# Performance work log

Measured on AMD Instinct MI355X. Metric: run time of the kernel, lower is better.

## Reference

```python
import jax, jax.numpy as jnp
import numpy as np

E = 1024        # embedding_dim
H = 16          # num_heads
DR = 1          # downsample_rate
INT = E // DR   # internal_dim
HD = INT // H   # head dim
B, NQ, NK = 4, 2048, 2048


def setup_inputs() -> dict:
    key = jax.random.key(0)
    ks = jax.random.split(key, 11)
    s_in = 1.0 / np.sqrt(E)
    s_int = 1.0 / np.sqrt(INT)
    return {
        "q": jax.random.normal(ks[0], (B, NQ, E), jnp.float32),
        "k": jax.random.normal(ks[1], (B, NK, E), jnp.float32),
        "v": jax.random.normal(ks[2], (B, NK, E), jnp.float32),
        "wq": jax.random.normal(ks[3], (E, INT), jnp.float32) * s_in,
        "bq": jnp.zeros((INT,), jnp.float32),
        "wk": jax.random.normal(ks[4], (E, INT), jnp.float32) * s_in,
        "bk": jnp.zeros((INT,), jnp.float32),
        "wv": jax.random.normal(ks[5], (E, INT), jnp.float32) * s_in,
        "bv": jnp.zeros((INT,), jnp.float32),
        "wo": jax.random.normal(ks[6], (INT, E), jnp.float32) * s_int,
        "bo": jnp.zeros((E,), jnp.float32),
    }


def _heads(x):
    # (B, N, INT) -> (B, H, N, HD)
    b, n, c = x.shape
    return x.reshape(b, n, H, c // H).transpose(0, 2, 1, 3)


def reference(q, k, v, wq, bq, wk, bk, wv, bv, wo, bo):
    qh = _heads(q @ wq + bq)          # (B,H,NQ,HD)
    kh = _heads(k @ wk + bk)          # (B,H,NK,HD)
    vh = _heads(v @ wv + bv)          # (B,H,NK,HD)
    scale = 1.0 / np.sqrt(HD)
    attn = jnp.einsum('bhqd,bhkd->bhqk', qh, kh) * scale  # (B,H,NQ,NK)
    attn = jax.nn.softmax(attn, axis=-1)
    out = jnp.einsum('bhqk,bhkd->bhqd', attn, vh)          # (B,H,NQ,HD)
    out = out.transpose(0, 2, 1, 3).reshape(q.shape[0], qh.shape[2], INT)
    return out @ wo + bo
```

## Files before the change

kernel.cpp:

```cpp
#include <hip/hip_runtime.h>
#include <hip/hip_bf16.h>
#include <cstdint>
#include <cstddef>

typedef __bf16 bf16_t;
typedef __bf16 bf16x8 __attribute__((ext_vector_type(8)));
typedef float f32x4 __attribute__((ext_vector_type(4)));
typedef float f32x16 __attribute__((ext_vector_type(16)));
typedef uint32_t u32;

#define EDIM 1024
#define HH 16
#define HD 64
#define NSEQ 2048
#define QSCALE 0.18033688011f

__device__ __forceinline__ void async_copy16(const bf16_t* gsrc, bf16_t* lds_dst) {
    __builtin_amdgcn_global_load_lds(
        (const __attribute__((address_space(1))) uint32_t*)gsrc,
        (__attribute__((address_space(3))) uint32_t*)lds_dst,
        16, 0, 0);
}

__global__ void cvt_f32_bf16(const float* __restrict__ in, bf16_t* __restrict__ out) {
    size_t i = ((size_t)blockIdx.x * 256 + threadIdx.x) * 8;
    float4 x = *(const float4*)(in + i);
    float4 y = *(const float4*)(in + i + 4);
    bf16x8 v = {(bf16_t)x.x, (bf16_t)x.y, (bf16_t)x.z, (bf16_t)x.w,
                (bf16_t)y.x, (bf16_t)y.y, (bf16_t)y.z, (bf16_t)y.w};
    *(bf16x8*)(out + i) = v;
}

__global__ void transpose_all(const float* __restrict__ w0, const float* __restrict__ w1,
                              const float* __restrict__ w2, const float* __restrict__ w3,
                              bf16_t* __restrict__ o0, bf16_t* __restrict__ o1,
                              bf16_t* __restrict__ o2, bf16_t* __restrict__ o3) {
    __shared__ bf16_t t[64][65];
    const float* in;
    bf16_t* out;
    switch (blockIdx.z) {
        case 0: in = w0; out = o0; break;
        case 1: in = w1; out = o1; break;
        case 2: in = w2; out = o2; break;
        default: in = w3; out = o3; break;
    }
    const int tid = threadIdx.x;
    const int kt = blockIdx.x, nt = blockIdx.y;
    #pragma unroll
    for (int i = 0; i < 16; i++) {
        int idx = i * 256 + tid;
        int r = idx >> 6, c = idx & 63;
        t[r][c] = (bf16_t)in[(size_t)(kt * 64 + r) * 1024 + nt * 64 + c];
    }
    __syncthreads();
    #pragma unroll
    for (int i = 0; i < 16; i++) {
        int idx = i * 256 + tid;
        int r = idx >> 6, c = idx & 63;
        out[(size_t)(nt * 64 + r) * 1024 + kt * 64 + c] = t[c][r];
    }
}

template <int AB, int MODE, typename OUT>
__global__ __launch_bounds__(256, 2)
void gemm_nt(const void* __restrict__ Araw, const bf16_t* __restrict__ Bt,
             const float* __restrict__ bias, OUT* __restrict__ C,
             int M, int N, int K, float oscale) {
    constexpr int BM = 128, BN = 128, BK = 32;
    __shared__ bf16_t Asm[BM * BK];
    __shared__ bf16_t Bsm[BN * BK];
    const int tid = threadIdx.x;
    const int wave = tid >> 6, lane = tid & 63;
    const int quad = lane >> 4, l15 = lane & 15;
    const int n0 = blockIdx.x * BN;
    const int m0 = blockIdx.y * BM;
    const int wm = (wave & 1) * 64, wn = (wave >> 1) * 64;

    f32x4 acc[4][4] = {};

    for (int k0 = 0; k0 < K; k0 += BK) {
        __syncthreads();
        if (AB) {
            const bf16_t* A = (const bf16_t*)Araw;
            #pragma unroll
            for (int i = 0; i < 2; i++) {
                int s = i * 256 + tid;
                int row = s >> 2, c = s & 3;
                int kc = c ^ ((row >> 1) & 3);
                async_copy16(A + (size_t)(m0 + row) * K + k0 + kc * 8, Asm + s * 8);
            }
        } else {
            const float* A = (const float*)Araw;
            #pragma unroll
            for (int i = 0; i < 2; i++) {
                int s = i * 256 + tid;
                int row = s >> 2, c = s & 3;
                int kc = c ^ ((row >> 1) & 3);
                const float* sp = A + (size_t)(m0 + row) * K + k0 + kc * 8;
                float4 x = *(const float4*)sp;
                float4 y = *(const float4*)(sp + 4);
                bf16x8 vv = {(bf16_t)x.x, (bf16_t)x.y, (bf16_t)x.z, (bf16_t)x.w,
                             (bf16_t)y.x, (bf16_t)y.y, (bf16_t)y.z, (bf16_t)y.w};
                *(bf16x8*)&Asm[s * 8] = vv;
            }
        }
        #pragma unroll
        for (int i = 0; i < 2; i++) {
            int s = i * 256 + tid;
            int row = s >> 2, c = s & 3;
            int kc = c ^ ((row >> 1) & 3);
            async_copy16(Bt + (size_t)(n0 + row) * K + k0 + kc * 8, Bsm + s * 8);
        }
        __syncthreads();

        bf16x8 af[4], bfr[4];
        #pragma unroll
        for (int mi = 0; mi < 4; mi++) {
            int row = wm + mi * 16 + l15;
            af[mi] = *(const bf16x8*)&Asm[row * BK + ((quad ^ ((row >> 1) & 3)) * 8)];
        }
        #pragma unroll
        for (int ni = 0; ni < 4; ni++) {
            int row = wn + ni * 16 + l15;
            bfr[ni] = *(const bf16x8*)&Bsm[row * BK + ((quad ^ ((row >> 1) & 3)) * 8)];
        }
        #pragma unroll
        for (int mi = 0; mi < 4; mi++)
            #pragma unroll
            for (int ni = 0; ni < 4; ni++)
                acc[mi][ni] = __builtin_amdgcn_mfma_f32_16x16x32_bf16(
                    af[mi], bfr[ni], acc[mi][ni], 0, 0, 0);
    }

    #pragma unroll
    for (int mi = 0; mi < 4; mi++) {
        #pragma unroll
        for (int ni = 0; ni < 4; ni++) {
            #pragma unroll
            for (int r = 0; r < 4; r++) {
                int m = m0 + wm + mi * 16 + quad * 4 + r;
                int nch = n0 + wn + ni * 16 + l15;
                float v = (acc[mi][ni][r] + bias[nch]) * oscale;
                if (MODE == 2) {
                    C[(size_t)m * N + nch] = (OUT)v;
                } else {
                    int b = m >> 11, n = m & 2047;
                    int h = nch >> 6, d = nch & 63;
                    if (MODE == 0)
                        C[(((size_t)(b * HH + h)) * NSEQ + n) * HD + d] = (OUT)v;
                    else
                        C[(((size_t)(b * HH + h)) * HD + d) * NSEQ + n] = (OUT)v;
                }
            }
        }
    }
}

union PW { u32 w[4]; bf16x8 v; };

__device__ __forceinline__ u32 pack_bf16(float lo, float hi) {
    union { bf16_t h[2]; u32 u; } x;
    x.h[0] = (bf16_t)lo;
    x.h[1] = (bf16_t)hi;
    return x.u;
}

__device__ __forceinline__ void half_swap(u32& a, u32& b, int hi) {
    u32 as = (u32)__shfl_xor((int)a, 32, 64);
    u32 bs = (u32)__shfl_xor((int)b, 32, 64);
    a = hi ? bs : a;
    b = hi ? b : as;
}

__device__ __forceinline__ void softmax_pack(const f32x16 sa, float* lp, int hi,
                                             PW& f0, PW& f1) {
    float p[16];
    #pragma unroll
    for (int r = 0; r < 16; r++) {
        p[r] = exp2f(sa[r]);
        lp[r & 3] += p[r];
    }
    u32 x0 = pack_bf16(p[0],  p[1]),  x1 = pack_bf16(p[2],  p[3]);
    u32 x2 = pack_bf16(p[4],  p[5]),  x3 = pack_bf16(p[6],  p[7]);
    u32 x4 = pack_bf16(p[8],  p[9]),  x5 = pack_bf16(p[10], p[11]);
    u32 x6 = pack_bf16(p[12], p[13]), x7 = pack_bf16(p[14], p[15]);
    half_swap(x0, x2, hi); half_swap(x1, x3, hi);
    half_swap(x4, x6, hi); half_swap(x5, x7, hi);
    f0.w[0] = x0; f0.w[1] = x1; f0.w[2] = x2; f0.w[3] = x3;
    f1.w[0] = x4; f1.w[1] = x5; f1.w[2] = x6; f1.w[3] = x7;
}

__global__ __launch_bounds__(256, 4)
void attn_kernel(const bf16_t* __restrict__ Qh, const bf16_t* __restrict__ Kh,
                 const bf16_t* __restrict__ Vt, bf16_t* __restrict__ out) {
    __shared__ bf16_t Ks[2][64 * 64];
    __shared__ bf16_t Vs[2][64 * 64];
    const int tid = threadIdx.x, wave = tid >> 6, lane = tid & 63;
    const int l31 = lane & 31, hi = lane >> 5;
    const int B = blockIdx.x;
    const int qt = (B >> 3) & 15;
    const int bh = (B >> 7) * 8 + (B & 7);
    const int b = bh >> 4, h = bh & 15;

    const bf16_t* kbase = Kh + (size_t)bh * NSEQ * HD;
    const bf16_t* vbase = Vt + (size_t)bh * HD * NSEQ;

    bf16x8 qf[4];
    {
        const bf16_t* qrow =
            Qh + ((size_t)bh * NSEQ + qt * 128 + wave * 32 + l31) * HD + hi * 8;
        #pragma unroll
        for (int s = 0; s < 4; s++) qf[s] = *(const bf16x8*)(qrow + s * 16);
    }

    const bf16_t *ks0, *ks1, *vs0, *vs1;
    {
        int r0 = tid >> 3, c0 = tid & 7;
        int s1 = tid + 256;
        int r1 = s1 >> 3, c1 = s1 & 7;
        ks0 = kbase + r0 * HD + (c0 ^ (r0 & 7)) * 8;
        ks1 = kbase + r1 * HD + (c1 ^ (r1 & 7)) * 8;
        vs0 = vbase + (size_t)r0 * NSEQ + (c0 ^ (r0 & 7)) * 8;
        vs1 = vbase + (size_t)r1 * NSEQ + (c1 ^ (r1 & 7)) * 8;
    }

    async_copy16(ks0, &Ks[0][tid * 8]);
    async_copy16(ks1, &Ks[0][(tid + 256) * 8]);
    async_copy16(vs0, &Vs[0][tid * 8]);
    async_copy16(vs1, &Vs[0][(tid + 256) * 8]);

    f32x16 oacc[2] = {};
    float lp[4] = {};

    for (int t = 0; t < 32; t++) {
        const int cur = t & 1;
        __syncthreads();

        if (t < 31) {
            ks0 += 64 * HD; ks1 += 64 * HD;
            vs0 += 64;      vs1 += 64;
            async_copy16(ks0, &Ks[cur ^ 1][tid * 8]);
            async_copy16(ks1, &Ks[cur ^ 1][(tid + 256) * 8]);
            async_copy16(vs0, &Vs[cur ^ 1][tid * 8]);
            async_copy16(vs1, &Vs[cur ^ 1][(tid + 256) * 8]);
        }

        f32x16 sacc0 = {};
        f32x16 sacc1 = {};
        #pragma unroll
        for (int s = 0; s < 4; s++) {
            int g = s * 2 + hi;
            int row0 = l31;
            int row1 = 32 + l31;
            bf16x8 ak0 = *(const bf16x8*)&Ks[cur][row0 * 64 + ((g ^ (row0 & 7)) * 8)];
            bf16x8 ak1 = *(const bf16x8*)&Ks[cur][row1 * 64 + ((g ^ (row1 & 7)) * 8)];
            sacc0 = __builtin_amdgcn_mfma_f32_32x32x16_bf16(ak0, qf[s], sacc0, 0, 0, 0);
            sacc1 = __builtin_amdgcn_mfma_f32_32x32x16_bf16(ak1, qf[s], sacc1, 0, 0, 0);
        }

        PW pa[4];
        softmax_pack(sacc0, lp, hi, pa[0], pa[1]);
        softmax_pack(sacc1, lp, hi, pa[2], pa[3]);

        #pragma unroll
        for (int dt = 0; dt < 2; dt++) {
            #pragma unroll
            for (int ks = 0; ks < 4; ks++) {
                int row = dt * 32 + l31;
                int g = ks * 2 + hi;
                bf16x8 bv = *(const bf16x8*)&Vs[cur][row * 64 + ((g ^ (row & 7)) * 8)];
                oacc[dt] = __builtin_amdgcn_mfma_f32_32x32x16_bf16(
                    pa[ks].v, bv, oacc[dt], 0, 0, 0);
            }
        }
    }

    float lsum = (lp[0] + lp[1]) + (lp[2] + lp[3]);
    lsum += __shfl_xor(lsum, 32, 64);
    float linv = 1.f / lsum;
    float rinv[16];
    #pragma unroll
    for (int r = 0; r < 16; r++) {
        int q = (r & 3) + 8 * (r >> 2) + 4 * hi;
        rinv[r] = __shfl(linv, q, 64);
    }

    const int n0 = qt * 128 + wave * 32;
    #pragma unroll
    for (int dt = 0; dt < 2; dt++) {
        int c = h * 64 + dt * 32 + l31;
        #pragma unroll
        for (int r = 0; r < 16; r++) {
            int q = (r & 3) + 8 * (r >> 2) + 4 * hi;
            out[((size_t)b * NSEQ + n0 + q) * EDIM + c] = (bf16_t)(oacc[dt][r] * rinv[r]);
        }
    }
}

extern "C" void kernel_launch(void* const* d_in, const int* in_sizes, int n_in,
                              void* d_out, int out_size, void* d_ws, size_t ws_size,
                              hipStream_t stream) {
    const float* q  = (const float*)d_in[0];
    const float* k  = (const float*)d_in[1];
    const float* v  = (const float*)d_in[2];
    const float* wq = (const float*)d_in[3];
    const float* bq = (const float*)d_in[4];
    const float* wk = (const float*)d_in[5];
    const float* bk = (const float*)d_in[6];
    const float* wv = (const float*)d_in[7];
    const float* bv = (const float*)d_in[8];
    const float* wo = (const float*)d_in[9];
    const float* bo = (const float*)d_in[10];
    float* out = (float*)d_out;

    char* ws = (char*)d_ws;
    bf16_t* wqt = (bf16_t*)(ws + ((size_t)0  << 20));
    bf16_t* wkt = (bf16_t*)(ws + ((size_t)2  << 20));
    bf16_t* wvt = (bf16_t*)(ws + ((size_t)4  << 20));
    bf16_t* wot = (bf16_t*)(ws + ((size_t)6  << 20));

    const bool big = ws_size >= ((size_t)90 << 20);
    size_t off = big ? ((size_t)24 << 20) : ((size_t)8 << 20);
    bf16_t* X   = (bf16_t*)(ws + ((size_t)8 << 20));
    bf16_t* Qh  = (bf16_t*)(ws + off);
    bf16_t* Kh  = (bf16_t*)(ws + off + ((size_t)16 << 20));
    bf16_t* Vt  = (bf16_t*)(ws + off + ((size_t)32 << 20));
    bf16_t* ao  = (bf16_t*)(ws + off + ((size_t)48 << 20));

    dim3 tb(256);

    transpose_all<<<dim3(16, 16, 4), tb, 0, stream>>>(wq, wk, wv, wo, wqt, wkt, wvt, wot);

    dim3 gg(8, 64);
    if (big) {
        cvt_f32_bf16<<<4096, tb, 0, stream>>>(q, X);
        gemm_nt<1, 0, bf16_t><<<gg, tb, 0, stream>>>(X, wqt, bq, Qh, 8192, 1024, 1024, QSCALE);
        cvt_f32_bf16<<<4096, tb, 0, stream>>>(k, X);
        gemm_nt<1, 0, bf16_t><<<gg, tb, 0, stream>>>(X, wkt, bk, Kh, 8192, 1024, 1024, 1.0f);
        cvt_f32_bf16<<<4096, tb, 0, stream>>>(v, X);
        gemm_nt<1, 1, bf16_t><<<gg, tb, 0, stream>>>(X, wvt, bv, Vt, 8192, 1024, 1024, 1.0f);
    } else {
        gemm_nt<0, 0, bf16_t><<<gg, tb, 0, stream>>>(q, wqt, bq, Qh, 8192, 1024, 1024, QSCALE);
        gemm_nt<0, 0, bf16_t><<<gg, tb, 0, stream>>>(k, wkt, bk, Kh, 8192, 1024, 1024, 1.0f);
        gemm_nt<0, 1, bf16_t><<<gg, tb, 0, stream>>>(v, wvt, bv, Vt, 8192, 1024, 1024, 1.0f);
    }

    attn_kernel<<<1024, tb, 0, stream>>>(Qh, Kh, Vt, ao);

    gemm_nt<1, 2, float><<<gg, tb, 0, stream>>>(ao, wot, bo, out, 8192, 1024, 1024, 1.0f);
}
```

Measured before the change: 397.8 us.

## Use permlane32_swap, native exp2, MFMA setprio, and relax launch bounds in attention

```diff
diff --git a/kernel.cpp b/kernel.cpp
--- a/kernel.cpp
+++ b/kernel.cpp
@@ -165,32 +165,31 @@
     return x.u;
 }
 
-__device__ __forceinline__ void half_swap(u32& a, u32& b, int hi) {
-    u32 as = (u32)__shfl_xor((int)a, 32, 64);
-    u32 bs = (u32)__shfl_xor((int)b, 32, 64);
-    a = hi ? bs : a;
-    b = hi ? b : as;
-}
-
-__device__ __forceinline__ void softmax_pack(const f32x16 sa, float* lp, int hi,
+__device__ __forceinline__ void half_swap(u32& a, u32& b) {
+    auto r = __builtin_amdgcn_permlane32_swap(a, b, false, false);
+    a = r[0];
+    b = r[1];
+}
+
+__device__ __forceinline__ void softmax_pack(const f32x16 sa, float* lp,
                                              PW& f0, PW& f1) {
     float p[16];
     #pragma unroll
     for (int r = 0; r < 16; r++) {
-        p[r] = exp2f(sa[r]);
+        p[r] = __builtin_amdgcn_exp2f(sa[r]);
         lp[r & 3] += p[r];
     }
     u32 x0 = pack_bf16(p[0],  p[1]),  x1 = pack_bf16(p[2],  p[3]);
     u32 x2 = pack_bf16(p[4],  p[5]),  x3 = pack_bf16(p[6],  p[7]);
     u32 x4 = pack_bf16(p[8],  p[9]),  x5 = pack_bf16(p[10], p[11]);
     u32 x6 = pack_bf16(p[12], p[13]), x7 = pack_bf16(p[14], p[15]);
-    half_swap(x0, x2, hi); half_swap(x1, x3, hi);
-    half_swap(x4, x6, hi); half_swap(x5, x7, hi);
+    half_swap(x0, x2); half_swap(x1, x3);
+    half_swap(x4, x6); half_swap(x5, x7);
     f0.w[0] = x0; f0.w[1] = x1; f0.w[2] = x2; f0.w[3] = x3;
     f1.w[0] = x4; f1.w[1] = x5; f1.w[2] = x6; f1.w[3] = x7;
 }
 
-__global__ __launch_bounds__(256, 4)
+__global__ __launch_bounds__(256, 2)
 void attn_kernel(const bf16_t* __restrict__ Qh, const bf16_t* __restrict__ Kh,
                  const bf16_t* __restrict__ Vt, bf16_t* __restrict__ out) {
     __shared__ bf16_t Ks[2][64 * 64];
@@ -245,22 +244,34 @@
             async_copy16(vs1, &Vs[cur ^ 1][(tid + 256) * 8]);
         }
 
-        f32x16 sacc0 = {};
-        f32x16 sacc1 = {};
-        #pragma unroll
-        for (int s = 0; s < 4; s++) {
+        const f32x16 zero = {};
+        f32x16 sacc0, sacc1;
+        {
+            int g = hi;
+            int row0 = l31, row1 = 32 + l31;
+            bf16x8 ak0 = *(const bf16x8*)&Ks[cur][row0 * 64 + ((g ^ (row0 & 7)) * 8)];
+            bf16x8 ak1 = *(const bf16x8*)&Ks[cur][row1 * 64 + ((g ^ (row1 & 7)) * 8)];
+            __builtin_amdgcn_s_setprio(1);
+            sacc0 = __builtin_amdgcn_mfma_f32_32x32x16_bf16(ak0, qf[0], zero, 0, 0, 0);
+            sacc1 = __builtin_amdgcn_mfma_f32_32x32x16_bf16(ak1, qf[0], zero, 0, 0, 0);
+            __builtin_amdgcn_s_setprio(0);
+        }
+        #pragma unroll
+        for (int s = 1; s < 4; s++) {
             int g = s * 2 + hi;
             int row0 = l31;
             int row1 = 32 + l31;
             bf16x8 ak0 = *(const bf16x8*)&Ks[cur][row0 * 64 + ((g ^ (row0 & 7)) * 8)];
             bf16x8 ak1 = *(const bf16x8*)&Ks[cur][row1 * 64 + ((g ^ (row1 & 7)) * 8)];
+            __builtin_amdgcn_s_setprio(1);
             sacc0 = __builtin_amdgcn_mfma_f32_32x32x16_bf16(ak0, qf[s], sacc0, 0, 0, 0);
             sacc1 = __builtin_amdgcn_mfma_f32_32x32x16_bf16(ak1, qf[s], sacc1, 0, 0, 0);
+            __builtin_amdgcn_s_setprio(0);
         }
 
         PW pa[4];
-        softmax_pack(sacc0, lp, hi, pa[0], pa[1]);
-        softmax_pack(sacc1, lp, hi, pa[2], pa[3]);
+        softmax_pack(sacc0, lp, pa[0], pa[1]);
+        softmax_pack(sacc1, lp, pa[2], pa[3]);
 
         #pragma unroll
         for (int dt = 0; dt < 2; dt++) {
@@ -269,8 +280,10 @@
                 int row = dt * 32 + l31;
                 int g = ks * 2 + hi;
                 bf16x8 bv = *(const bf16x8*)&Vs[cur][row * 64 + ((g ^ (row & 7)) * 8)];
+                __builtin_amdgcn_s_setprio(1);
                 oacc[dt] = __builtin_amdgcn_mfma_f32_32x32x16_bf16(
                     pa[ks].v, bv, oacc[dt], 0, 0, 0);
+                __builtin_amdgcn_s_setprio(0);
             }
         }
     }
```

New measurement: 371.2 us. 1.07x faster.
